# Kernel optimization log

Measured on AMD Instinct MI355X. Metric: run time of the kernel, lower is better.

## Reference

```python
import jax, jax.numpy as jnp
import numpy as np

DIM = 4096
N_HEADS = 32
HEAD_DIM = DIM // N_HEADS
BATCH = 2
SEQ = 1024
THETA = 10000.0
NEG_INF = -1e9


def _rope_cos_sin(seq_len, head_dim):
    # NOTE: original code constructs RotatePosEmbedding with config.dim but applies
    # it per-head; the only shape-consistent interpretation (standard Llama RoPE)
    # uses head_dim frequencies, which is what we implement.
    inv_freq = 1.0 / (THETA ** (jnp.arange(0, head_dim, 2, dtype=jnp.float32) / head_dim))
    angles = jnp.arange(seq_len, dtype=jnp.float32)[:, None] * inv_freq[None, :]  # [S, hd/2]
    return jnp.cos(angles), jnp.sin(angles)


def _apply_rope(x, cos, sin):
    # x: [B,S,H,hd]; rotate consecutive pairs (complex multiply)
    B, S, H, hd = x.shape
    xr = x.reshape(B, S, H, hd // 2, 2)
    x0, x1 = xr[..., 0], xr[..., 1]
    c = cos[None, :, None, :]
    s = sin[None, :, None, :]
    out = jnp.stack([x0 * c - x1 * s, x0 * s + x1 * c], axis=-1)
    return out.reshape(B, S, H, hd)


def setup_inputs() -> dict:
    key = jax.random.key(0)
    ks = jax.random.split(key, 9)
    x = jax.random.normal(ks[0], (BATCH, SEQ, DIM), dtype=jnp.float32)
    scale = 1.0 / np.sqrt(DIM)
    wq = jax.random.normal(ks[1], (DIM, DIM), dtype=jnp.float32) * scale
    wk = jax.random.normal(ks[2], (DIM, DIM), dtype=jnp.float32) * scale
    wv = jax.random.normal(ks[3], (DIM, DIM), dtype=jnp.float32) * scale
    wo = jax.random.normal(ks[4], (DIM, DIM), dtype=jnp.float32) * scale
    bq = jax.random.normal(ks[5], (DIM,), dtype=jnp.float32) * 0.01
    bk = jax.random.normal(ks[6], (DIM,), dtype=jnp.float32) * 0.01
    bv = jax.random.normal(ks[7], (DIM,), dtype=jnp.float32) * 0.01
    bo = jax.random.normal(ks[8], (DIM,), dtype=jnp.float32) * 0.01
    # causal additive mask [S,S]
    mask = jnp.where(jnp.tril(jnp.ones((SEQ, SEQ), dtype=bool)), 0.0, NEG_INF).astype(jnp.float32)
    return {"x": x, "wq": wq, "bq": bq, "wk": wk, "bk": bk, "wv": wv, "bv": bv,
            "wo": wo, "bo": bo, "mask": mask, "start_pos": 0}


def reference(x, wq, bq, wk, bk, wv, bv, wo, bo, mask, start_pos):
    B, S, D = x.shape
    H, hd = N_HEADS, D // N_HEADS
    q = (x @ wq.T + bq).reshape(B, S, H, hd)
    k = (x @ wk.T + bk).reshape(B, S, H, hd)
    v = (x @ wv.T + bv).reshape(B, S, H, hd)
    cos, sin = _rope_cos_sin(S, hd)
    q = _apply_rope(q, cos, sin)
    k = _apply_rope(k, cos, sin)
    # start_pos == 0 prefill: cache slice [:start_pos+S] equals current k/v
    scores = jnp.einsum('bqhd,bkhd->bhqk', q, k) / np.sqrt(hd).astype(np.float32)
    scores = scores + mask[None, None, :, :]
    attn = jax.nn.softmax(scores, axis=-1)
    out = jnp.einsum('bhqk,bkhd->bqhd', attn, v).reshape(B, S, D)
    return out @ wo.T + bo
```

## Files before the change

### kernel.cpp

```cpp
#include <hip/hip_runtime.h>
#include <hip/hip_bf16.h>

#define DIM   4096
#define NH    32
#define HD    128
#define BATCH 2
#define SEQ   1024
#define MROWS (BATCH*SEQ)
#define LDQ   12288

typedef __attribute__((ext_vector_type(8))) short bf16x8;
typedef __attribute__((ext_vector_type(4))) short s16x4;
typedef __attribute__((ext_vector_type(4))) float f32x4;

__device__ inline void gload_lds16(const void* g, void* l) {
  __builtin_amdgcn_global_load_lds(
      (const __attribute__((address_space(1))) void*)g,
      (__attribute__((address_space(3))) void*)l, 16, 0, 0);
}

__device__ inline float bf2f(short b) {
  unsigned u = ((unsigned)(unsigned short)b) << 16;
  return __uint_as_float(u);
}
__device__ inline unsigned short f2bfu(float f) {
  __hip_bfloat16 h = __float2bfloat16(f);
  return *reinterpret_cast<unsigned short*>(&h);
}

__global__ void cvt_all_kernel(const float* __restrict__ x, const float* __restrict__ wq,
                               const float* __restrict__ wk, const float* __restrict__ wv,
                               const float* __restrict__ wo,
                               unsigned short* __restrict__ xb,
                               unsigned short* __restrict__ wqkvb,
                               unsigned short* __restrict__ wob) {
  const long NW = 4l << 20;
  const long NX = 2l << 20;
  const long total = NX + 4 * NW;
  long i = blockIdx.x * (long)blockDim.x + threadIdx.x;
  long stride = (long)gridDim.x * blockDim.x;
  for (; i < total; i += stride) {
    const float* src; unsigned short* dst; long off;
    if (i < NX) { src = x; dst = xb; off = i; }
    else {
      long j = i - NX;
      int wsel = (int)(j >> 22);
      off = j & (NW - 1);
      if (wsel == 0)      { src = wq; dst = wqkvb; }
      else if (wsel == 1) { src = wk; dst = wqkvb + (size_t)DIM * DIM; }
      else if (wsel == 2) { src = wv; dst = wqkvb + 2 * (size_t)DIM * DIM; }
      else                { src = wo; dst = wob; }
    }
    float4 v = ((const float4*)src)[off];
    ushort4 o;
    o.x = f2bfu(v.x); o.y = f2bfu(v.y); o.z = f2bfu(v.z); o.w = f2bfu(v.w);
    ((ushort4*)dst)[off] = o;
  }
}

__global__ void concat3_kernel(const float* __restrict__ a, const float* __restrict__ b,
                               const float* __restrict__ c, float* __restrict__ o) {
  int i = blockIdx.x * blockDim.x + threadIdx.x;
  if (i < 4096) o[i] = a[i];
  else if (i < 8192) o[i] = b[i - 4096];
  else if (i < 12288) o[i] = c[i - 8192];
}

__global__ void rope_table_kernel(float* __restrict__ cosT, float* __restrict__ sinT) {
  int s = blockIdx.x;
  int p = threadIdx.x;
  float inv = powf(10000.0f, -((float)(2 * p)) / 128.0f);
  float a = (float)s * inv;
  cosT[s * 64 + p] = cosf(a);
  sinT[s * 64 + p] = sinf(a);
}

template <typename OutT, bool ROPE>
__global__ __launch_bounds__(256, 2) void gemm_m97p_kernel(
    const unsigned short* __restrict__ A, const unsigned short* __restrict__ Bw,
    const float* __restrict__ bias, OutT* __restrict__ C,
    int M, int N, int Kstr,
    const float* __restrict__ cosT, const float* __restrict__ sinT) {
  __shared__ unsigned short As[3][128 * 32];
  __shared__ unsigned short Bs[3][128 * 32];
  const int t = threadIdx.x;
  const int lane = t & 63;
  const int w = t >> 6;
  const int wm = w >> 1, wn = w & 1;
  const int np = lane & 15, hq = lane >> 4;
  const int kc = ((hq ^ ((np >> 1) & 3)) << 3);

  int bid = blockIdx.y * gridDim.x + blockIdx.x;
  int k = bid & 7;
  int local = bid >> 3;
  int sw = gridDim.x >> 3;
  int bx = k * sw + local / gridDim.y;
  int by = local % gridDim.y;
  const int m0 = by * 128, n0 = bx * 128;
  const int H = Kstr >> 5;

  auto stage = [&](int slot, int kcol0) {
#pragma unroll
    for (int j = 0; j < 2; ++j) {
      int ci = j * 256 + t;
      int r = ci >> 2, p = ci & 3, g = p ^ ((r >> 1) & 3);
      gload_lds16(A + (size_t)(m0 + r) * Kstr + kcol0 + g * 8, &As[slot][ci * 8]);
    }
#pragma unroll
    for (int j = 0; j < 2; ++j) {
      int ci = j * 256 + t;
      int r = ci >> 2, p = ci & 3, g = p ^ ((r >> 1) & 3);
      gload_lds16(Bw + (size_t)(n0 + r) * Kstr + kcol0 + g * 8, &Bs[slot][ci * 8]);
    }
  };

  stage(0, 0); stage(1, 32);
  asm volatile("s_waitcnt vmcnt(4)" ::: "memory");
  __builtin_amdgcn_s_barrier();

  f32x4 acc[4][4] = {};

  int sl = 0;
#pragma unroll 1
  for (int u = 0; u < H; ++u) {
    const unsigned short* Asl = As[sl];
    const unsigned short* Bsl = Bs[sl];
    bf16x8 af[4], bfr[4];
#pragma unroll
    for (int i = 0; i < 4; ++i)
      af[i] = *(const bf16x8*)&Asl[(wm * 64 + i * 16 + np) * 32 + kc];
#pragma unroll
    for (int j = 0; j < 4; ++j)
      bfr[j] = *(const bf16x8*)&Bsl[(wn * 64 + j * 16 + np) * 32 + kc];

    if (u + 2 < H) {
      int ssl = sl + 2; if (ssl >= 3) ssl -= 3;
      stage(ssl, (u + 2) << 5);
    }

    __builtin_amdgcn_s_setprio(1);
#pragma unroll
    for (int i = 0; i < 4; ++i)
#pragma unroll
      for (int j = 0; j < 4; ++j)
        acc[i][j] = __builtin_amdgcn_mfma_f32_16x16x32_bf16(af[i], bfr[j], acc[i][j], 0, 0, 0);
    __builtin_amdgcn_s_setprio(0);

    if (u + 1 < H) {
      if (u + 2 < H) asm volatile("s_waitcnt vmcnt(4)" ::: "memory");
      else           asm volatile("s_waitcnt vmcnt(0)" ::: "memory");
      __builtin_amdgcn_s_barrier();
    }
    sl = (sl == 2) ? 0 : sl + 1;
  }

  const int orow0 = m0 + wm * 64;
  const int ocol0 = n0 + wn * 64 + np;
#pragma unroll
  for (int j = 0; j < 4; ++j) {
    const int col = ocol0 + j * 16;
    float bj = bias[col];
    const int p0 = (col & 127) >> 1;
    const bool even = (lane & 1) == 0;
    const bool do_rope = ROPE && (col < 8192);
#pragma unroll
    for (int i = 0; i < 4; ++i) {
#pragma unroll
      for (int r = 0; r < 4; ++r) {
        int orow = orow0 + i * 16 + hq * 4 + r;
        float v = acc[i][j][r] + bj;
        float pv = __shfl_xor(v, 1);
        if (do_rope) {
          int srow = orow & (SEQ - 1);
          float c = cosT[srow * 64 + p0];
          float s = sinT[srow * 64 + p0];
          v = even ? (v * c - pv * s) : (pv * s + v * c);
        }
        size_t off = (size_t)orow * N + col;
        if constexpr (sizeof(OutT) == 2)
          ((unsigned short*)C)[off] = f2bfu(v);
        else
          ((float*)C)[off] = v;
      }
    }
  }
}

__global__ __launch_bounds__(256, 1) void flash_attn_kernel(
    const unsigned short* __restrict__ QKV, unsigned short* __restrict__ O) {
  __shared__ unsigned short Ks[64 * 128];
  __shared__ unsigned short Vt[128 * 64];
  __shared__ unsigned short Ps[4][32 * 64];

  const int p  = blockIdx.x;
  const int bh = blockIdx.y;
  const int b  = bh >> 5;
  const int hh = bh & 31;
  const int t    = threadIdx.x;
  const int lane = t & 63;
  const int w    = t >> 6;
  const int np   = lane & 15;
  const int hq   = lane >> 4;

  const size_t rowbase = (size_t)b * SEQ * LDQ;
  const unsigned short* Qg = QKV + rowbase + (size_t)hh * HD;
  const unsigned short* Kg = QKV + rowbase + 4096 + (size_t)hh * HD;
  const unsigned short* Vg = QKV + rowbase + 8192 + (size_t)hh * HD;
  unsigned short* Og = O + (size_t)b * SEQ * DIM + (size_t)hh * HD;

  const int krow = t >> 2;
  const int kc0  = (t & 3) * 32;
  const int vr0  = (t & 15) * 4;
  const int vc0  = (t >> 4) * 8;

  unsigned short* Pw = &Ps[w][0];
  const float SCALE = 0.08838834764831843f;

  bf16x8 vk[4], vv[4];

#pragma unroll 1
  for (int pass = 0; pass < 2; ++pass) {
    const int qt    = pass ? (7 - p) : p;
    const int nt    = 2 * qt + 2;
    const int qbase = qt * 128 + w * 32;

    bf16x8 qf[2][4];
#pragma unroll
    for (int rb = 0; rb < 2; ++rb)
#pragma unroll
      for (int kb = 0; kb < 4; ++kb)
        qf[rb][kb] = *(const bf16x8*)&Qg[(size_t)(qbase + rb * 16 + np) * LDQ + kb * 32 + hq * 8];

    f32x4 acc[2][8] = {};
    float m_run[2][4], l_run[2][4];
#pragma unroll
    for (int rb = 0; rb < 2; ++rb)
#pragma unroll
      for (int r = 0; r < 4; ++r) { m_run[rb][r] = -3.0e38f; l_run[rb][r] = 0.0f; }

    {
      const unsigned short* kp = Kg + (size_t)krow * LDQ + kc0;
      const unsigned short* vp = Vg + (size_t)vr0 * LDQ + vc0;
#pragma unroll
      for (int jj = 0; jj < 4; ++jj) vk[jj] = *(const bf16x8*)(kp + jj * 8);
#pragma unroll
      for (int jj = 0; jj < 4; ++jj) vv[jj] = *(const bf16x8*)(vp + (size_t)jj * LDQ);
    }

#pragma unroll 1
    for (int kt = 0; kt < nt; ++kt) {
      __syncthreads();

#pragma unroll
      for (int jj = 0; jj < 4; ++jj) {
        int c = (t & 3) * 4 + jj;
        *(bf16x8*)((char*)Ks + krow * 256 + ((c ^ (krow & 7)) << 4)) = vk[jj];
      }
#pragma unroll
      for (int i = 0; i < 8; ++i) {
        int col = vc0 + i;
        s16x4 sv;
        sv[0] = vv[0][i]; sv[1] = vv[1][i]; sv[2] = vv[2][i]; sv[3] = vv[3][i];
        *(s16x4*)((char*)Vt + ((col * 128 + vr0 * 2) ^ ((col & 7) << 4))) = sv;
      }
      __syncthreads();

      if (kt + 1 < nt) {
        const unsigned short* kp = Kg + (size_t)((kt + 1) * 64 + krow) * LDQ + kc0;
        const unsigned short* vp = Vg + (size_t)((kt + 1) * 64 + vr0) * LDQ + vc0;
#pragma unroll
        for (int jj = 0; jj < 4; ++jj) vk[jj] = *(const bf16x8*)(kp + jj * 8);
#pragma unroll
        for (int jj = 0; jj < 4; ++jj) vv[jj] = *(const bf16x8*)(vp + (size_t)jj * LDQ);
      }

      f32x4 sc[4][2] = {};
#pragma unroll
      for (int ct = 0; ct < 4; ++ct) {
#pragma unroll
        for (int kb = 0; kb < 4; ++kb) {
          bf16x8 kf = *(const bf16x8*)((char*)Ks + (ct * 16 + np) * 256 +
                                       (((kb * 4 + hq) ^ (np & 7)) << 4));
          sc[ct][0] = __builtin_amdgcn_mfma_f32_16x16x32_bf16(qf[0][kb], kf, sc[ct][0], 0, 0, 0);
          sc[ct][1] = __builtin_amdgcn_mfma_f32_16x16x32_bf16(qf[1][kb], kf, sc[ct][1], 0, 0, 0);
        }
      }

      const bool maskt = (kt >= 2 * qt);
#pragma unroll
      for (int ct = 0; ct < 4; ++ct) {
        int kvc = kt * 64 + ct * 16 + np;
#pragma unroll
        for (int rb = 0; rb < 2; ++rb)
#pragma unroll
          for (int r = 0; r < 4; ++r) {
            float v = sc[ct][rb][r] * SCALE;
            if (maskt && kvc > qbase + rb * 16 + hq * 4 + r) v = -1.0e9f;
            sc[ct][rb][r] = v;
          }
      }

      float sf[2][4];
#pragma unroll
      for (int rb = 0; rb < 2; ++rb)
#pragma unroll
        for (int r = 0; r < 4; ++r) {
          float tmax = fmaxf(fmaxf(sc[0][rb][r], sc[1][rb][r]),
                             fmaxf(sc[2][rb][r], sc[3][rb][r]));
          tmax = fmaxf(tmax, __shfl_xor(tmax, 1));
          tmax = fmaxf(tmax, __shfl_xor(tmax, 2));
          tmax = fmaxf(tmax, __shfl_xor(tmax, 4));
          tmax = fmaxf(tmax, __shfl_xor(tmax, 8));
          float mn = fmaxf(m_run[rb][r], tmax);
          sf[rb][r] = __expf(m_run[rb][r] - mn);
          m_run[rb][r] = mn;
        }

#pragma unroll
      for (int rb = 0; rb < 2; ++rb)
#pragma unroll
        for (int r = 0; r < 4; ++r) {
          int prow = rb * 16 + hq * 4 + r;
          int swz = (prow & 7) << 4;
          float rsum = 0.f;
#pragma unroll
          for (int ct = 0; ct < 4; ++ct) {
            float pv = __expf(sc[ct][rb][r] - m_run[rb][r]);
            rsum += pv;
            *(unsigned short*)((char*)Pw + ((prow * 128 + (ct * 16 + np) * 2) ^ swz)) = f2bfu(pv);
          }
          rsum += __shfl_xor(rsum, 1);
          rsum += __shfl_xor(rsum, 2);
          rsum += __shfl_xor(rsum, 4);
          rsum += __shfl_xor(rsum, 8);
          l_run[rb][r] = l_run[rb][r] * sf[rb][r] + rsum;
        }

#pragma unroll
      for (int rb = 0; rb < 2; ++rb)
#pragma unroll
        for (int nt2 = 0; nt2 < 8; ++nt2)
#pragma unroll
          for (int r = 0; r < 4; ++r)
            acc[rb][nt2][r] *= sf[rb][r];

#pragma unroll
      for (int kb2 = 0; kb2 < 2; ++kb2) {
        bf16x8 pa0 = *(const bf16x8*)((char*)Pw +
            (((0 * 16 + np) * 128 + kb2 * 64 + hq * 16) ^ ((np & 7) << 4)));
        bf16x8 pa1 = *(const bf16x8*)((char*)Pw +
            (((1 * 16 + np) * 128 + kb2 * 64 + hq * 16) ^ ((np & 7) << 4)));
#pragma unroll
        for (int nt2 = 0; nt2 < 8; ++nt2) {
          int col = nt2 * 16 + np;
          bf16x8 vf = *(const bf16x8*)((char*)Vt +
              ((col * 128 + kb2 * 64 + hq * 16) ^ ((col & 7) << 4)));
          acc[0][nt2] = __builtin_amdgcn_mfma_f32_16x16x32_bf16(pa0, vf, acc[0][nt2], 0, 0, 0);
          acc[1][nt2] = __builtin_amdgcn_mfma_f32_16x16x32_bf16(pa1, vf, acc[1][nt2], 0, 0, 0);
        }
      }
    }

#pragma unroll
    for (int rb = 0; rb < 2; ++rb)
#pragma unroll
      for (int r = 0; r < 4; ++r) {
        float rl = 1.0f / l_run[rb][r];
        int orow = qbase + rb * 16 + hq * 4 + r;
#pragma unroll
        for (int nt2 = 0; nt2 < 8; ++nt2)
          Og[(size_t)orow * DIM + nt2 * 16 + np] = f2bfu(acc[rb][nt2][r] * rl);
      }
  }
}

extern "C" void kernel_launch(void* const* d_in, const int* in_sizes, int n_in,
                              void* d_out, int out_size, void* d_ws, size_t ws_size,
                              hipStream_t stream) {
  const float* x  = (const float*)d_in[0];
  const float* wq = (const float*)d_in[1];
  const float* bq = (const float*)d_in[2];
  const float* wk = (const float*)d_in[3];
  const float* bk = (const float*)d_in[4];
  const float* wv = (const float*)d_in[5];
  const float* bv = (const float*)d_in[6];
  const float* wo = (const float*)d_in[7];
  const float* bo = (const float*)d_in[8];
  float* out = (float*)d_out;

  char* ws = (char*)d_ws;
  unsigned short* wqkvb = (unsigned short*)(ws);
  unsigned short* wob   = (unsigned short*)(ws + (96ll  << 20));
  unsigned short* xb    = (unsigned short*)(ws + (128ll << 20));
  unsigned short* qkv   = (unsigned short*)(ws + (144ll << 20));
  unsigned short* ab    = (unsigned short*)(ws + (192ll << 20));
  float* biasqkv = (float*)(ws + (208ll << 20));
  float* cosT    = (float*)(ws + (208ll << 20) + (64  << 10));
  float* sinT    = (float*)(ws + (208ll << 20) + (320 << 10));

  cvt_all_kernel<<<4096, 256, 0, stream>>>(x, wq, wk, wv, wo, xb, wqkvb, wob);

  concat3_kernel<<<48, 256, 0, stream>>>(bq, bk, bv, biasqkv);
  rope_table_kernel<<<SEQ, 64, 0, stream>>>(cosT, sinT);

  dim3 gq(LDQ / 128, MROWS / 128);
  gemm_m97p_kernel<unsigned short, true><<<gq, 256, 0, stream>>>(
      xb, wqkvb, biasqkv, qkv, MROWS, LDQ, DIM, cosT, sinT);

  dim3 ga(4, BATCH * NH);
  flash_attn_kernel<<<ga, 256, 0, stream>>>(qkv, ab);

  dim3 go(DIM / 128, MROWS / 128);
  gemm_m97p_kernel<float, false><<<go, 256, 0, stream>>>(
      ab, wob, bo, out, MROWS, DIM, DIM, nullptr, nullptr);
}
```

Before: 520.3 us.

## Fuse fp32 weight-to-bf16 conversion into GEMM B-tile staging, drop separate convert pass

Removes the upfront weight conversion kernel and the bias concat. The GEMMs now read fp32 weights directly into registers, convert them to bf16 and write them to LDS through a register double-buffer, while A still uses async global-to-LDS loads. This avoids writing and re-reading about 128MB of bf16 weights per call. In exchange, each weight tile is reconverted by every M-tile block and twice as many bytes are fetched per B tile, adding VGPR pressure and synchronous LDS writes in the main loop.

```diff
diff --git a/kernel.cpp b/kernel.cpp
--- a/kernel.cpp
+++ b/kernel.cpp
@@ -28,42 +28,14 @@
   return *reinterpret_cast<unsigned short*>(&h);
 }
 
-__global__ void cvt_all_kernel(const float* __restrict__ x, const float* __restrict__ wq,
-                               const float* __restrict__ wk, const float* __restrict__ wv,
-                               const float* __restrict__ wo,
-                               unsigned short* __restrict__ xb,
-                               unsigned short* __restrict__ wqkvb,
-                               unsigned short* __restrict__ wob) {
-  const long NW = 4l << 20;
-  const long NX = 2l << 20;
-  const long total = NX + 4 * NW;
+__global__ void cvt_x_kernel(const float* __restrict__ in,
+                             unsigned short* __restrict__ out) {
   long i = blockIdx.x * (long)blockDim.x + threadIdx.x;
-  long stride = (long)gridDim.x * blockDim.x;
-  for (; i < total; i += stride) {
-    const float* src; unsigned short* dst; long off;
-    if (i < NX) { src = x; dst = xb; off = i; }
-    else {
-      long j = i - NX;
-      int wsel = (int)(j >> 22);
-      off = j & (NW - 1);
-      if (wsel == 0)      { src = wq; dst = wqkvb; }
-      else if (wsel == 1) { src = wk; dst = wqkvb + (size_t)DIM * DIM; }
-      else if (wsel == 2) { src = wv; dst = wqkvb + 2 * (size_t)DIM * DIM; }
-      else                { src = wo; dst = wob; }
-    }
-    float4 v = ((const float4*)src)[off];
-    ushort4 o;
-    o.x = f2bfu(v.x); o.y = f2bfu(v.y); o.z = f2bfu(v.z); o.w = f2bfu(v.w);
-    ((ushort4*)dst)[off] = o;
-  }
-}
-
-__global__ void concat3_kernel(const float* __restrict__ a, const float* __restrict__ b,
-                               const float* __restrict__ c, float* __restrict__ o) {
-  int i = blockIdx.x * blockDim.x + threadIdx.x;
-  if (i < 4096) o[i] = a[i];
-  else if (i < 8192) o[i] = b[i - 4096];
-  else if (i < 12288) o[i] = c[i - 8192];
+  if (i >= (long)MROWS * DIM / 4) return;
+  float4 v = ((const float4*)in)[i];
+  ushort4 o;
+  o.x = f2bfu(v.x); o.y = f2bfu(v.y); o.z = f2bfu(v.z); o.w = f2bfu(v.w);
+  ((ushort4*)out)[i] = o;
 }
 
 __global__ void rope_table_kernel(float* __restrict__ cosT, float* __restrict__ sinT) {
@@ -76,10 +48,13 @@
 }
 
 template <typename OutT, bool ROPE>
-__global__ __launch_bounds__(256, 2) void gemm_m97p_kernel(
-    const unsigned short* __restrict__ A, const unsigned short* __restrict__ Bw,
-    const float* __restrict__ bias, OutT* __restrict__ C,
-    int M, int N, int Kstr,
+__global__ __launch_bounds__(256, 2) void gemm_f32b_kernel(
+    const unsigned short* __restrict__ A,
+    const float* __restrict__ W0, const float* __restrict__ W1,
+    const float* __restrict__ W2,
+    const float* __restrict__ b0, const float* __restrict__ b1,
+    const float* __restrict__ b2,
+    OutT* __restrict__ C, int M, int N, int Kstr,
     const float* __restrict__ cosT, const float* __restrict__ sinT) {
   __shared__ unsigned short As[3][128 * 32];
   __shared__ unsigned short Bs[3][128 * 32];
@@ -99,32 +74,58 @@
   const int m0 = by * 128, n0 = bx * 128;
   const int H = Kstr >> 5;
 
-  auto stage = [&](int slot, int kcol0) {
+  const float* Bw   = (n0 < 4096) ? W0 : (n0 < 8192 ? W1 : W2);
+  const float* bias = (n0 < 4096) ? b0 : (n0 < 8192 ? b1 : b2);
+  const int nr0 = n0 & 4095;
+
+  auto stageA = [&](int slot, int kcol0) {
 #pragma unroll
     for (int j = 0; j < 2; ++j) {
       int ci = j * 256 + t;
       int r = ci >> 2, p = ci & 3, g = p ^ ((r >> 1) & 3);
       gload_lds16(A + (size_t)(m0 + r) * Kstr + kcol0 + g * 8, &As[slot][ci * 8]);
     }
+  };
+  auto loadB = [&](float4 (&d)[4], int kcol0) {
 #pragma unroll
     for (int j = 0; j < 2; ++j) {
       int ci = j * 256 + t;
       int r = ci >> 2, p = ci & 3, g = p ^ ((r >> 1) & 3);
-      gload_lds16(Bw + (size_t)(n0 + r) * Kstr + kcol0 + g * 8, &Bs[slot][ci * 8]);
+      const float* src = Bw + (size_t)(nr0 + r) * Kstr + kcol0 + g * 8;
+      d[2 * j]     = *(const float4*)(src);
+      d[2 * j + 1] = *(const float4*)(src + 4);
     }
   };
-
-  stage(0, 0); stage(1, 32);
-  asm volatile("s_waitcnt vmcnt(4)" ::: "memory");
+  auto writeB = [&](int slot, const float4 (&s)[4]) {
+#pragma unroll
+    for (int j = 0; j < 2; ++j) {
+      int ci = j * 256 + t;
+      bf16x8 o;
+      o[0] = (short)f2bfu(s[2 * j].x);     o[1] = (short)f2bfu(s[2 * j].y);
+      o[2] = (short)f2bfu(s[2 * j].z);     o[3] = (short)f2bfu(s[2 * j].w);
+      o[4] = (short)f2bfu(s[2 * j + 1].x); o[5] = (short)f2bfu(s[2 * j + 1].y);
+      o[6] = (short)f2bfu(s[2 * j + 1].z); o[7] = (short)f2bfu(s[2 * j + 1].w);
+      *(bf16x8*)&Bs[slot][ci * 8] = o;
+    }
+  };
+
+  float4 bst0[4], bst1[4];
+
+  stageA(0, 0);  loadB(bst0, 0);
+  stageA(1, 32); loadB(bst1, 32);
+  writeB(0, bst0);
+  asm volatile("s_waitcnt vmcnt(0)" ::: "memory");
+  asm volatile("s_waitcnt lgkmcnt(0)" ::: "memory");
   __builtin_amdgcn_s_barrier();
 
   f32x4 acc[4][4] = {};
-
   int sl = 0;
-#pragma unroll 1
-  for (int u = 0; u < H; ++u) {
+
+  auto phase = [&](int u, float4 (&wrt)[4], float4 (&lod)[4]) {
     const unsigned short* Asl = As[sl];
     const unsigned short* Bsl = Bs[sl];
+    int sl1 = sl + 1; if (sl1 >= 3) sl1 -= 3;
+    int sl2 = sl1 + 1; if (sl2 >= 3) sl2 -= 3;
     bf16x8 af[4], bfr[4];
 #pragma unroll
     for (int i = 0; i < 4; ++i)
@@ -133,10 +134,7 @@
     for (int j = 0; j < 4; ++j)
       bfr[j] = *(const bf16x8*)&Bsl[(wn * 64 + j * 16 + np) * 32 + kc];
 
-    if (u + 2 < H) {
-      int ssl = sl + 2; if (ssl >= 3) ssl -= 3;
-      stage(ssl, (u + 2) << 5);
-    }
+    if (u + 2 < H) { stageA(sl2, (u + 2) << 5); loadB(lod, (u + 2) << 5); }
 
     __builtin_amdgcn_s_setprio(1);
 #pragma unroll
@@ -147,22 +145,31 @@
     __builtin_amdgcn_s_setprio(0);
 
     if (u + 1 < H) {
-      if (u + 2 < H) asm volatile("s_waitcnt vmcnt(4)" ::: "memory");
+      writeB(sl1, wrt);
+      if (u + 2 < H) asm volatile("s_waitcnt vmcnt(6)" ::: "memory");
       else           asm volatile("s_waitcnt vmcnt(0)" ::: "memory");
+      asm volatile("s_waitcnt lgkmcnt(0)" ::: "memory");
+      __builtin_amdgcn_sched_barrier(0);
       __builtin_amdgcn_s_barrier();
     }
-    sl = (sl == 2) ? 0 : sl + 1;
+    sl = sl1;
+  };
+
+#pragma unroll 1
+  for (int u = 0; u < H; u += 2) {
+    phase(u, bst1, bst0);
+    phase(u + 1, bst0, bst1);
   }
 
   const int orow0 = m0 + wm * 64;
   const int ocol0 = n0 + wn * 64 + np;
+  const bool do_rope = ROPE && (n0 < 8192);
 #pragma unroll
   for (int j = 0; j < 4; ++j) {
     const int col = ocol0 + j * 16;
-    float bj = bias[col];
+    float bj = bias[col & 4095];
     const int p0 = (col & 127) >> 1;
     const bool even = (lane & 1) == 0;
-    const bool do_rope = ROPE && (col < 8192);
 #pragma unroll
     for (int i = 0; i < 4; ++i) {
 #pragma unroll
@@ -389,28 +396,23 @@
   float* out = (float*)d_out;
 
   char* ws = (char*)d_ws;
-  unsigned short* wqkvb = (unsigned short*)(ws);
-  unsigned short* wob   = (unsigned short*)(ws + (96ll  << 20));
-  unsigned short* xb    = (unsigned short*)(ws + (128ll << 20));
-  unsigned short* qkv   = (unsigned short*)(ws + (144ll << 20));
-  unsigned short* ab    = (unsigned short*)(ws + (192ll << 20));
-  float* biasqkv = (float*)(ws + (208ll << 20));
-  float* cosT    = (float*)(ws + (208ll << 20) + (64  << 10));
-  float* sinT    = (float*)(ws + (208ll << 20) + (320 << 10));
-
-  cvt_all_kernel<<<4096, 256, 0, stream>>>(x, wq, wk, wv, wo, xb, wqkvb, wob);
-
-  concat3_kernel<<<48, 256, 0, stream>>>(bq, bk, bv, biasqkv);
+  unsigned short* xb  = (unsigned short*)(ws);
+  unsigned short* qkv = (unsigned short*)(ws + (16ll << 20));
+  unsigned short* ab  = (unsigned short*)(ws + (64ll << 20));
+  float* cosT = (float*)(ws + (80ll << 20));
+  float* sinT = (float*)(ws + (80ll << 20) + (256 << 10));
+
+  cvt_x_kernel<<<(MROWS * DIM / 4 + 255) / 256, 256, 0, stream>>>(x, xb);
   rope_table_kernel<<<SEQ, 64, 0, stream>>>(cosT, sinT);
 
   dim3 gq(LDQ / 128, MROWS / 128);
-  gemm_m97p_kernel<unsigned short, true><<<gq, 256, 0, stream>>>(
-      xb, wqkvb, biasqkv, qkv, MROWS, LDQ, DIM, cosT, sinT);
+  gemm_f32b_kernel<unsigned short, true><<<gq, 256, 0, stream>>>(
+      xb, wq, wk, wv, bq, bk, bv, qkv, MROWS, LDQ, DIM, cosT, sinT);
 
   dim3 ga(4, BATCH * NH);
   flash_attn_kernel<<<ga, 256, 0, stream>>>(qkv, ab);
 
   dim3 go(DIM / 128, MROWS / 128);
-  gemm_m97p_kernel<float, false><<<go, 256, 0, stream>>>(
-      ab, wob, bo, out, MROWS, DIM, DIM, nullptr, nullptr);
-}
+  gemm_f32b_kernel<float, false><<<go, 256, 0, stream>>>(
+      ab, wo, wo, wo, bo, bo, bo, out, MROWS, DIM, DIM, nullptr, nullptr);
+}
```

Result: slower. 567.1 us (+9.0%).

## Deepen GEMM LDS pipeline to four stages and fuse prep kernels

Applied to the files above, without the earlier changes.

The bf16 GEMM now keeps four LDS buffers and prefetches three K-tiles ahead instead of two, with vmcnt waits adjusted to match, to hide more global-load latency. The bias concat and RoPE table kernels are merged into the conversion kernel, removing two launches. LDS per block grows from 48KB to 64KB, which may limit occupancy under the launch bound of two blocks per CU.

```diff
diff --git a/kernel.cpp b/kernel.cpp
--- a/kernel.cpp
+++ b/kernel.cpp
@@ -28,51 +28,54 @@
   return *reinterpret_cast<unsigned short*>(&h);
 }
 
-__global__ void cvt_all_kernel(const float* __restrict__ x, const float* __restrict__ wq,
-                               const float* __restrict__ wk, const float* __restrict__ wv,
-                               const float* __restrict__ wo,
-                               unsigned short* __restrict__ xb,
-                               unsigned short* __restrict__ wqkvb,
-                               unsigned short* __restrict__ wob) {
+__global__ void prep_kernel(const float* __restrict__ x, const float* __restrict__ wq,
+                            const float* __restrict__ wk, const float* __restrict__ wv,
+                            const float* __restrict__ wo,
+                            const float* __restrict__ bq, const float* __restrict__ bk,
+                            const float* __restrict__ bv,
+                            unsigned short* __restrict__ xb,
+                            unsigned short* __restrict__ wqkvb,
+                            unsigned short* __restrict__ wob,
+                            float* __restrict__ biasqkv,
+                            float* __restrict__ cosT, float* __restrict__ sinT) {
+  const long NB = 12288;
+  const long NR = 65536;
+  const long NX = 2l << 20;
   const long NW = 4l << 20;
-  const long NX = 2l << 20;
-  const long total = NX + 4 * NW;
+  const long total = NB + NR + NX + 4 * NW;
   long i = blockIdx.x * (long)blockDim.x + threadIdx.x;
   long stride = (long)gridDim.x * blockDim.x;
   for (; i < total; i += stride) {
-    const float* src; unsigned short* dst; long off;
-    if (i < NX) { src = x; dst = xb; off = i; }
-    else {
-      long j = i - NX;
-      int wsel = (int)(j >> 22);
-      off = j & (NW - 1);
-      if (wsel == 0)      { src = wq; dst = wqkvb; }
-      else if (wsel == 1) { src = wk; dst = wqkvb + (size_t)DIM * DIM; }
-      else if (wsel == 2) { src = wv; dst = wqkvb + 2 * (size_t)DIM * DIM; }
-      else                { src = wo; dst = wob; }
-    }
-    float4 v = ((const float4*)src)[off];
-    ushort4 o;
-    o.x = f2bfu(v.x); o.y = f2bfu(v.y); o.z = f2bfu(v.z); o.w = f2bfu(v.w);
-    ((ushort4*)dst)[off] = o;
+    if (i < NB) {
+      int j = (int)i;
+      float v = (j < 4096) ? bq[j] : (j < 8192 ? bk[j - 4096] : bv[j - 8192]);
+      biasqkv[j] = v;
+    } else if (i < NB + NR) {
+      int j = (int)(i - NB);
+      int s = j >> 6, p = j & 63;
+      float inv = powf(10000.0f, -((float)(2 * p)) / 128.0f);
+      float a = (float)s * inv;
+      cosT[j] = cosf(a);
+      sinT[j] = sinf(a);
+    } else {
+      long j = i - NB - NR;
+      const float* src; unsigned short* dst; long off;
+      if (j < NX) { src = x; dst = xb; off = j; }
+      else {
+        long q = j - NX;
+        int wsel = (int)(q >> 22);
+        off = q & (NW - 1);
+        if (wsel == 0)      { src = wq; dst = wqkvb; }
+        else if (wsel == 1) { src = wk; dst = wqkvb + (size_t)DIM * DIM; }
+        else if (wsel == 2) { src = wv; dst = wqkvb + 2 * (size_t)DIM * DIM; }
+        else                { src = wo; dst = wob; }
+      }
+      float4 v = ((const float4*)src)[off];
+      ushort4 o;
+      o.x = f2bfu(v.x); o.y = f2bfu(v.y); o.z = f2bfu(v.z); o.w = f2bfu(v.w);
+      ((ushort4*)dst)[off] = o;
+    }
   }
-}
-
-__global__ void concat3_kernel(const float* __restrict__ a, const float* __restrict__ b,
-                               const float* __restrict__ c, float* __restrict__ o) {
-  int i = blockIdx.x * blockDim.x + threadIdx.x;
-  if (i < 4096) o[i] = a[i];
-  else if (i < 8192) o[i] = b[i - 4096];
-  else if (i < 12288) o[i] = c[i - 8192];
-}
-
-__global__ void rope_table_kernel(float* __restrict__ cosT, float* __restrict__ sinT) {
-  int s = blockIdx.x;
-  int p = threadIdx.x;
-  float inv = powf(10000.0f, -((float)(2 * p)) / 128.0f);
-  float a = (float)s * inv;
-  cosT[s * 64 + p] = cosf(a);
-  sinT[s * 64 + p] = sinf(a);
 }
 
 template <typename OutT, bool ROPE>
@@ -81,8 +84,8 @@
     const float* __restrict__ bias, OutT* __restrict__ C,
     int M, int N, int Kstr,
     const float* __restrict__ cosT, const float* __restrict__ sinT) {
-  __shared__ unsigned short As[3][128 * 32];
-  __shared__ unsigned short Bs[3][128 * 32];
+  __shared__ unsigned short As[4][128 * 32];
+  __shared__ unsigned short Bs[4][128 * 32];
   const int t = threadIdx.x;
   const int lane = t & 63;
   const int w = t >> 6;
@@ -114,17 +117,16 @@
     }
   };
 
-  stage(0, 0); stage(1, 32);
-  asm volatile("s_waitcnt vmcnt(4)" ::: "memory");
+  stage(0, 0); stage(1, 32); stage(2, 64);
+  asm volatile("s_waitcnt vmcnt(8)" ::: "memory");
   __builtin_amdgcn_s_barrier();
 
   f32x4 acc[4][4] = {};
 
-  int sl = 0;
 #pragma unroll 1
   for (int u = 0; u < H; ++u) {
-    const unsigned short* Asl = As[sl];
-    const unsigned short* Bsl = Bs[sl];
+    const unsigned short* Asl = As[u & 3];
+    const unsigned short* Bsl = Bs[u & 3];
     bf16x8 af[4], bfr[4];
 #pragma unroll
     for (int i = 0; i < 4; ++i)
@@ -133,10 +135,7 @@
     for (int j = 0; j < 4; ++j)
       bfr[j] = *(const bf16x8*)&Bsl[(wn * 64 + j * 16 + np) * 32 + kc];
 
-    if (u + 2 < H) {
-      int ssl = sl + 2; if (ssl >= 3) ssl -= 3;
-      stage(ssl, (u + 2) << 5);
-    }
+    if (u + 3 < H) stage((u + 3) & 3, (u + 3) << 5);
 
     __builtin_amdgcn_s_setprio(1);
 #pragma unroll
@@ -147,11 +146,12 @@
     __builtin_amdgcn_s_setprio(0);
 
     if (u + 1 < H) {
-      if (u + 2 < H) asm volatile("s_waitcnt vmcnt(4)" ::: "memory");
-      else           asm volatile("s_waitcnt vmcnt(0)" ::: "memory");
+      int rem = (u + 2 < H ? 1 : 0) + (u + 3 < H ? 1 : 0);
+      if (rem == 2)      asm volatile("s_waitcnt vmcnt(8)" ::: "memory");
+      else if (rem == 1) asm volatile("s_waitcnt vmcnt(4)" ::: "memory");
+      else               asm volatile("s_waitcnt vmcnt(0)" ::: "memory");
       __builtin_amdgcn_s_barrier();
     }
-    sl = (sl == 2) ? 0 : sl + 1;
   }
 
   const int orow0 = m0 + wm * 64;
@@ -398,10 +398,8 @@
   float* cosT    = (float*)(ws + (208ll << 20) + (64  << 10));
   float* sinT    = (float*)(ws + (208ll << 20) + (320 << 10));
 
-  cvt_all_kernel<<<4096, 256, 0, stream>>>(x, wq, wk, wv, wo, xb, wqkvb, wob);
-
-  concat3_kernel<<<48, 256, 0, stream>>>(bq, bk, bv, biasqkv);
-  rope_table_kernel<<<SEQ, 64, 0, stream>>>(cosT, sinT);
+  prep_kernel<<<4096, 256, 0, stream>>>(x, wq, wk, wv, wo, bq, bk, bv,
+                                        xb, wqkvb, wob, biasqkv, cosT, sinT);
 
   dim3 gq(LDQ / 128, MROWS / 128);
   gemm_m97p_kernel<unsigned short, true><<<gq, 256, 0, stream>>>(
```

Result: slower. 552.7 us (+6.2%).
